# Kernel tuning notes

Hardware: AMD Instinct MI355X
Metric: run time of the kernel (lower is better)

Reference implementation:

```python
import jax, jax.numpy as jnp
import numpy as np
import math

D_MODEL = 1024
N_HEADS = 16
HEAD_DIM = D_MODEL // N_HEADS  # 64
B, T = 2, 2048


def _rotate_half(x):
    x1, x2 = jnp.split(x, 2, axis=-1)
    return jnp.concatenate([-x2, x1], axis=-1)


def _rope_sin_cos(seq_len, dim, dtype=jnp.float32):
    # matches RotaryEmbedding: inv_freq over even indices, emb = [freqs, freqs]
    inv_freq = 1.0 / (10000.0 ** (jnp.arange(0, dim, 2, dtype=dtype) / dim))
    t = jnp.arange(seq_len, dtype=dtype)
    freqs = jnp.einsum('i,j->ij', t, inv_freq)          # [T, dim/2]
    emb = jnp.concatenate((freqs, freqs), axis=-1)      # [T, dim]
    sin = jnp.sin(emb)[None, :, None, :]                # [1, T, 1, dim]
    cos = jnp.cos(emb)[None, :, None, :]
    return sin, cos


def setup_inputs() -> dict:
    key = jax.random.key(0)
    k1, k2, k3 = jax.random.split(key, 3)
    x = jax.random.normal(k1, (B, T, D_MODEL), dtype=jnp.float32)
    # causal mask broadcast over batch and heads: [1, 1, T, T]
    mask = jnp.tril(jnp.ones((T, T), dtype=bool))[None, None]
    w_qkv = jax.random.normal(k2, (D_MODEL, 3 * D_MODEL), dtype=jnp.float32) / math.sqrt(D_MODEL)
    w_out = jax.random.normal(k3, (D_MODEL, D_MODEL), dtype=jnp.float32) / math.sqrt(D_MODEL)
    return {"x": x, "mask": mask, "w_qkv": w_qkv, "w_out": w_out}


def reference(x, mask, w_qkv, w_out):
    Bx, Tx, Dx = x.shape
    qkv = x @ w_qkv                                     # [B, T, 3D]
    q, k, v = jnp.split(qkv, 3, axis=-1)
    q = q.reshape(Bx, Tx, N_HEADS, HEAD_DIM)
    k = k.reshape(Bx, Tx, N_HEADS, HEAD_DIM)
    v = v.reshape(Bx, Tx, N_HEADS, HEAD_DIM)
    sin, cos = _rope_sin_cos(Tx, HEAD_DIM, x.dtype)
    q = q * cos + _rotate_half(q) * sin
    k = k * cos + _rotate_half(k) * sin
    scores = jnp.einsum('bthd,bThd->bhtT', q, k) / math.sqrt(HEAD_DIM)
    scores = jnp.where(mask, scores, -1e10)
    probs = jax.nn.softmax(scores, axis=-1)             # [B, H, T, T]
    out = jnp.einsum('bhtT,bThd->bthd', probs, v)
    out = out.reshape(Bx, Tx, Dx)
    return out @ w_out
```

## Files before the change

### kernel.cpp

```cpp
#include <hip/hip_runtime.h>
#include <math.h>

typedef unsigned short u16;
typedef __attribute__((ext_vector_type(8))) short short8;
typedef __attribute__((ext_vector_type(4))) float f32x4;

__device__ __forceinline__ u16 f2bf(float f) {
  unsigned int u = __float_as_uint(f);
  u += 0x7fffu + ((u >> 16) & 1u);
  return (u16)(u >> 16);
}
__device__ __forceinline__ float bf2f(u16 h) {
  return __uint_as_float(((unsigned int)h) << 16);
}

__device__ __forceinline__ f32x4 mfma16(short8 a, short8 b, f32x4 c) {
  return __builtin_amdgcn_mfma_f32_16x16x32_bf16(a, b, c, 0, 0, 0);
}

__device__ __forceinline__ unsigned cvtpk_bf16(float lo, float hi) {
  unsigned r;
  asm("v_cvt_pk_bf16_f32 %0, %1, %2" : "=v"(r) : "v"(lo), "v"(hi));
  return r;
}

__device__ __forceinline__ float fexp2(float x) {
  float r;
  asm("v_exp_f32 %0, %1" : "=v"(r) : "v"(x));
  return r;
}

#define QSCL 0.18033688011112042f
#define EXPB 11.541560327111707f

#define NEG_BIG (-1e30f)

__device__ __forceinline__ void glds16(const u16* g, u16* l) {
  __builtin_amdgcn_global_load_lds(
      (const __attribute__((address_space(1))) unsigned int*)g,
      (__attribute__((address_space(3))) unsigned int*)l, 16, 0, 0);
}

__global__ __launch_bounds__(256) void detect_dtype3(const u16* __restrict__ a,
                                                     const u16* __restrict__ bb,
                                                     const u16* __restrict__ c,
                                                     int* __restrict__ flags) {
  const u16* x = (blockIdx.x == 0) ? a : (blockIdx.x == 1) ? bb : c;
  __shared__ int cnt;
  if (threadIdx.x == 0) cnt = 0;
  __syncthreads();
  int my = 0;
  for (int i = threadIdx.x; i < 4096; i += 256) {
    float v = bf2f(x[2 * i]);
    float av = fabsf(v);
    if (v == 0.0f || (av >= 1e-4f && av <= 100.0f)) my++;
  }
  atomicAdd(&cnt, my);
  __syncthreads();
  if (threadIdx.x == 0) flags[blockIdx.x] = (cnt > 2458) ? 1 : 0;
}

__global__ __launch_bounds__(256) void prep_all(const void* __restrict__ wqkv,
                                                const void* __restrict__ wout,
                                                const void* __restrict__ xin,
                                                u16* __restrict__ wqkvT,
                                                u16* __restrict__ woutT,
                                                u16* __restrict__ xb,
                                                float2* __restrict__ tab,
                                                const int* __restrict__ flags) {
  int z = blockIdx.z;
  int tid = threadIdx.x;
  if (z == 2) {
    if (blockIdx.x >= 16 || blockIdx.y >= 16) return;
    int idx = (blockIdx.y * 16 + blockIdx.x) * 256 + tid;
    int t = idx >> 5, d = idx & 31;
    float invf = expf(-(float)d * 0.28782313662425575f);
    float s, c;
    sincosf((float)t * invf, &s, &c);
    tab[idx] = make_float2(c, s);
    return;
  }
  if (z == 3) {
    bool isbf = (flags[0] != 0);
    int tg = (blockIdx.y * 48 + blockIdx.x) * 256 + tid;
    for (int i = tg; i < 524288; i += 196608) {
      int base = i * 8;
      if (isbf) {
        *(short8*)(xb + base) = *(const short8*)((const u16*)xin + base);
      } else {
        const float* xf = (const float*)xin;
        f32x4 x0 = *(const f32x4*)(xf + base);
        f32x4 x1 = *(const f32x4*)(xf + base + 4);
        short8 o;
#pragma unroll
        for (int u = 0; u < 4; ++u) { o[u] = (short)f2bf(x0[u]); o[u + 4] = (short)f2bf(x1[u]); }
        *(short8*)(xb + base) = o;
      }
    }
    return;
  }
  const void* in = (z == 0) ? wqkv : wout;
  u16* out = (z == 0) ? wqkvT : woutT;
  int C = (z == 0) ? 3072 : 1024;
  const int R = 1024;
  bool isbf = (flags[z + 1] != 0);
  if (z == 1 && blockIdx.x >= 16) return;
  __shared__ float tile[64][68];
  int tc = blockIdx.x * 64, tr = blockIdx.y * 64;
  int r = tid >> 3, cg = (tid & 7) << 3;
#pragma unroll
  for (int p = 0; p < 2; ++p) {
    int row = r + p * 32;
    if (isbf) {
      short8 v = *(const short8*)((const u16*)in + (size_t)(tr + row) * C + tc + cg);
#pragma unroll
      for (int u = 0; u < 8; ++u) tile[row][cg + u] = bf2f((u16)v[u]);
    } else {
      const float* inf = (const float*)in + (size_t)(tr + row) * C + tc + cg;
#pragma unroll
      for (int u = 0; u < 8; ++u) tile[row][cg + u] = inf[u];
    }
  }
  __syncthreads();
#pragma unroll
  for (int p = 0; p < 2; ++p) {
    int orow = r + p * 32;
    short8 v;
#pragma unroll
    for (int u = 0; u < 8; ++u) v[u] = (short)f2bf(tile[cg + u][orow]);
    *(short8*)(out + (size_t)(tc + orow) * R + tr + cg) = v;
  }
}

__device__ __forceinline__ void qkv_epilogue3(f32x4 acc[4][4], int bm, int bn,
                                              int wm, int wn, int quad, int lane15,
                                              int lane, const float2* __restrict__ tab,
                                              u16* Qo, u16* Ko, u16* VTo, u16* myE) {
  int nbase = bn + wn * 64;
  int h = (nbase & 1023) >> 6;
  if (nbase < 2048) {
    float qs = (nbase < 1024) ? QSCL : 1.0f;
    int l8 = lane15 & 7, lh = lane15 >> 3;
#pragma unroll
    for (int i = 0; i < 4; ++i) {
#pragma unroll
      for (int r = 0; r < 4; ++r) {
        int mloc = i * 16 + quad * 4 + r;
        int t = (bm + wm * 64 + mloc) & 2047;
        float2 cs0 = tab[t * 32 + lane15];
        float2 cs1 = tab[t * 32 + 16 + lane15];
        float v0 = acc[i][0][r], v1 = acc[i][1][r], v2 = acc[i][2][r], v3 = acc[i][3][r];
        int m7 = mloc & 7;
        u16* rowp = myE + mloc * 64 + l8;
        rowp[((0 + lh) ^ m7) * 8] = f2bf(qs * (v0 * cs0.x - v2 * cs0.y));
        rowp[((2 + lh) ^ m7) * 8] = f2bf(qs * (v1 * cs1.x - v3 * cs1.y));
        rowp[((4 + lh) ^ m7) * 8] = f2bf(qs * (v2 * cs0.x + v0 * cs0.y));
        rowp[((6 + lh) ^ m7) * 8] = f2bf(qs * (v3 * cs1.x + v1 * cs1.y));
      }
    }
    asm volatile("s_waitcnt lgkmcnt(0)" ::: "memory");
    u16* dst = (nbase < 1024) ? Qo : Ko;
#pragma unroll
    for (int p = 0; p < 8; ++p) {
      int f = p * 64 + lane;
      int mr = f >> 3, nc = f & 7;
      short8 val = *(const short8*)(myE + mr * 64 + (nc ^ (mr & 7)) * 8);
      int g = bm + wm * 64 + mr;
      int bI = g >> 11, tI = g & 2047;
      *(short8*)(dst + ((size_t)(bI * 16 + h) * 2048 + tI) * 64 + nc * 8) = val;
    }
  } else {
#pragma unroll
    for (int i = 0; i < 4; ++i)
#pragma unroll
      for (int j = 0; j < 4; ++j)
#pragma unroll
        for (int r = 0; r < 4; ++r) {
          int col = i * 16 + quad * 4 + r;
          int slot = (col >> 3) ^ (lane15 & 7);
          myE[(j * 16 + lane15) * 64 + slot * 8 + (col & 7)] = f2bf(acc[i][j][r]);
        }
    asm volatile("s_waitcnt lgkmcnt(0)" ::: "memory");
    int g0 = bm + wm * 64;
    int bI = g0 >> 11, t0 = g0 & 2047;
#pragma unroll
    for (int p = 0; p < 8; ++p) {
      int f = p * 64 + lane;
      int dr = f >> 3, tc = f & 7;
      short8 val = *(const short8*)(myE + dr * 64 + (tc ^ (dr & 7)) * 8);
      *(short8*)(VTo + ((size_t)(bI * 16 + h) * 64 + dr) * 2048 + t0 + tc * 8) = val;
    }
  }
}

__device__ __forceinline__ void stage256(const u16* __restrict__ X,
                                         const u16* __restrict__ WT,
                                         u16* lAq, u16* lBq,
                                         int bm, int bn, int k0, int tid) {
  const int K = 1024;
#pragma unroll
  for (int p = 0; p < 4; ++p) {
    int cid = p * 512 + tid;
    int r = cid >> 3;
    int cs = (cid & 7) ^ (r & 7);
    int dst = (cid & ~63) * 8;
    glds16(X + (size_t)(bm + r) * K + k0 + cs * 8, lAq + dst);
    glds16(WT + (size_t)(bn + r) * K + k0 + cs * 8, lBq + dst);
  }
}

__device__ __forceinline__ void qkv_step(const u16* lAq, const u16* lBq,
                                         f32x4 acc[8][4], int wm, int wn,
                                         int lane15, int quad) {
  short8 bfr[2][4];
#pragma unroll
  for (int j = 0; j < 4; ++j) {
    int row = wn * 64 + j * 16 + lane15;
    int ro = row * 64, r7 = row & 7;
    bfr[0][j] = *(const short8*)(lBq + ro + (quad ^ r7) * 8);
    bfr[1][j] = *(const short8*)(lBq + ro + ((4 + quad) ^ r7) * 8);
  }
#pragma unroll
  for (int qd = 0; qd < 4; ++qd) {
    short8 afr[2][2];
#pragma unroll
    for (int i2 = 0; i2 < 2; ++i2) {
      int row = wm * 128 + (qd * 2 + i2) * 16 + lane15;
      int ro = row * 64, r7 = row & 7;
      afr[i2][0] = *(const short8*)(lAq + ro + (quad ^ r7) * 8);
      afr[i2][1] = *(const short8*)(lAq + ro + ((4 + quad) ^ r7) * 8);
    }
    __builtin_amdgcn_s_setprio(1);
#pragma unroll
    for (int ks = 0; ks < 2; ++ks)
#pragma unroll
      for (int i2 = 0; i2 < 2; ++i2)
#pragma unroll
        for (int j = 0; j < 4; ++j)
          acc[qd * 2 + i2][j] = mfma16(afr[i2][ks], bfr[ks][j], acc[qd * 2 + i2][j]);
    __builtin_amdgcn_s_setprio(0);
  }
}

__global__ __launch_bounds__(512, 2) void gemm_qkv_256(const u16* __restrict__ X,
                                                       const u16* __restrict__ WT,
                                                       const float2* __restrict__ tab,
                                                       u16* __restrict__ Qo,
                                                       u16* __restrict__ Ko,
                                                       u16* __restrict__ VTo) {
  __shared__ u16 sh[65536];
  int tid = threadIdx.x;
  int wave = tid >> 6, lane = tid & 63;
  int lane15 = lane & 15, quad = lane >> 4;
  int wm = wave >> 2, wn = wave & 3;
  int swz = (blockIdx.x & 7) * 24 + (blockIdx.x >> 3);
  int bm = (swz / 12) * 256, bn = (swz % 12) * 256;
  f32x4 acc[8][4] = {};

  stage256(X, WT, sh, sh + 32768, bm, bn, 0, tid);

#pragma unroll 1
  for (int kt = 0; kt < 15; ++kt) {
    int q = kt & 1;
    stage256(X, WT, sh + (q ^ 1) * 16384, sh + 32768 + (q ^ 1) * 16384,
             bm, bn, (kt + 1) * 64, tid);
    asm volatile("s_waitcnt vmcnt(8)" ::: "memory");
    __builtin_amdgcn_sched_barrier(0);
    asm volatile("s_barrier" ::: "memory");
    qkv_step(sh + q * 16384, sh + 32768 + q * 16384, acc, wm, wn, lane15, quad);
    asm volatile("s_barrier" ::: "memory");
  }
  asm volatile("s_waitcnt vmcnt(0)" ::: "memory");
  __builtin_amdgcn_sched_barrier(0);
  asm volatile("s_barrier" ::: "memory");
  qkv_step(sh + 16384, sh + 32768 + 16384, acc, wm, wn, lane15, quad);
  __syncthreads();

  u16* myE = sh + wave * 8192;
  int nbase = bn + wn * 64;
  int h = (nbase & 1023) >> 6;
  if (nbase < 2048) {
    float qs = (nbase < 1024) ? QSCL : 1.0f;
    int l8 = lane15 & 7, lh = lane15 >> 3;
#pragma unroll
    for (int i = 0; i < 8; ++i) {
#pragma unroll
      for (int r = 0; r < 4; ++r) {
        int mloc = i * 16 + quad * 4 + r;
        int t = (bm + wm * 128 + mloc) & 2047;
        float2 cs0 = tab[t * 32 + lane15];
        float2 cs1 = tab[t * 32 + 16 + lane15];
        float v0 = acc[i][0][r], v1 = acc[i][1][r], v2 = acc[i][2][r], v3 = acc[i][3][r];
        int m7 = mloc & 7;
        u16* rowp = myE + mloc * 64 + l8;
        rowp[((0 + lh) ^ m7) * 8] = f2bf(qs * (v0 * cs0.x - v2 * cs0.y));
        rowp[((2 + lh) ^ m7) * 8] = f2bf(qs * (v1 * cs1.x - v3 * cs1.y));
        rowp[((4 + lh) ^ m7) * 8] = f2bf(qs * (v2 * cs0.x + v0 * cs0.y));
        rowp[((6 + lh) ^ m7) * 8] = f2bf(qs * (v3 * cs1.x + v1 * cs1.y));
      }
    }
    asm volatile("s_waitcnt lgkmcnt(0)" ::: "memory");
    u16* dst = (nbase < 1024) ? Qo : Ko;
#pragma unroll
    for (int p = 0; p < 16; ++p) {
      int f = p * 64 + lane;
      int mr = f >> 3, nc = f & 7;
      short8 val = *(const short8*)(myE + mr * 64 + (nc ^ (mr & 7)) * 8);
      int g = bm + wm * 128 + mr;
      int bI = g >> 11, tI = g & 2047;
      *(short8*)(dst + ((size_t)(bI * 16 + h) * 2048 + tI) * 64 + nc * 8) = val;
    }
  } else {
#pragma unroll
    for (int i = 0; i < 8; ++i)
#pragma unroll
      for (int j = 0; j < 4; ++j)
#pragma unroll
        for (int r = 0; r < 4; ++r) {
          int col = i * 16 + quad * 4 + r;
          int slot = (col >> 3) ^ (lane15 & 7);
          myE[(j * 16 + lane15) * 128 + slot * 8 + (col & 7)] = f2bf(acc[i][j][r]);
        }
    asm volatile("s_waitcnt lgkmcnt(0)" ::: "memory");
    int g0 = bm + wm * 128;
    int bI = g0 >> 11, t0 = g0 & 2047;
#pragma unroll
    for (int p = 0; p < 16; ++p) {
      int f = p * 64 + lane;
      int dr = f >> 4, tc = f & 15;
      short8 val = *(const short8*)(myE + dr * 128 + (tc ^ (dr & 7)) * 8);
      *(short8*)(VTo + ((size_t)(bI * 16 + h) * 64 + dr) * 2048 + t0 + tc * 8) = val;
    }
  }
}

__global__ __launch_bounds__(256) void gemm_qkv_rope(const void* __restrict__ Xv,
                                                     const u16* __restrict__ WT,
                                                     const float2* __restrict__ tab,
                                                     u16* __restrict__ Qo,
                                                     u16* __restrict__ Ko,
                                                     u16* __restrict__ VTo,
                                                     const int* __restrict__ flag) {
  const int K = 1024;
  __shared__ u16 buf[16384];
  u16* lA = buf;
  u16* lB = buf + 5120;
  bool isbf = (*flag != 0);
  int tid = threadIdx.x;
  int wave = tid >> 6, lane = tid & 63;
  int lane15 = lane & 15, quad = lane >> 4;
  int wm = wave >> 1, wn = wave & 1;
  int bm = blockIdx.x * 128, bn = blockIdx.y * 128;
  int sr = tid >> 2, scg = (tid & 3) << 3;
  f32x4 acc[4][4] = {};
  for (int k0 = 0; k0 < K; k0 += 32) {
    __syncthreads();
#pragma unroll
    for (int p = 0; p < 2; ++p) {
      int row = sr + p * 64;
      if (isbf) {
        *(short8*)(lA + row * 40 + scg) =
            *(const short8*)((const u16*)Xv + (size_t)(bm + row) * K + k0 + scg);
      } else {
        const float* xf = (const float*)Xv + (size_t)(bm + row) * K + k0 + scg;
        f32x4 x0 = *(const f32x4*)(xf);
        f32x4 x1 = *(const f32x4*)(xf + 4);
        short8 o;
#pragma unroll
        for (int u = 0; u < 4; ++u) { o[u] = (short)f2bf(x0[u]); o[u + 4] = (short)f2bf(x1[u]); }
        *(short8*)(lA + row * 40 + scg) = o;
      }
      *(short8*)(lB + row * 40 + scg) = *(const short8*)(WT + (size_t)(bn + row) * K + k0 + scg);
    }
    __syncthreads();
    short8 af[4], bf[4];
#pragma unroll
    for (int i = 0; i < 4; ++i)
      af[i] = *(const short8*)(lA + (wm * 64 + i * 16 + lane15) * 40 + quad * 8);
#pragma unroll
    for (int j = 0; j < 4; ++j)
      bf[j] = *(const short8*)(lB + (wn * 64 + j * 16 + lane15) * 40 + quad * 8);
#pragma unroll
    for (int i = 0; i < 4; ++i)
#pragma unroll
      for (int j = 0; j < 4; ++j)
        acc[i][j] = mfma16(af[i], bf[j], acc[i][j]);
  }
  __syncthreads();
  qkv_epilogue3(acc, bm, bn, wm, wn, quad, lane15, lane, tab, Qo, Ko, VTo,
                buf + wave * 4096);
}

__device__ __forceinline__ short8 lds_frag(const u16* buf, int row, int chunk) {
  int s = chunk ^ (row & 7);
  return *(const short8*)(buf + row * 64 + s * 8);
}

__device__ __forceinline__ void stage_tile(const u16* gK, const u16* gV,
                                           u16* lK, u16* lV, int wave, int lane) {
#pragma unroll
  for (int p = 0; p < 2; ++p) {
    int f = (p * 4 + wave) * 64 + lane;
    int r = f >> 3;
    int c = (f & 7) ^ (r & 7);
    glds16(gK + (size_t)r * 64 + c * 8, lK + (p * 4 + wave) * 512);
    glds16(gV + (size_t)r * 2048 + c * 8, lV + (p * 4 + wave) * 512);
  }
}

__global__ __launch_bounds__(256, 4) void attn_fused(const u16* __restrict__ Q,
                                                     const u16* __restrict__ K,
                                                     const u16* __restrict__ VT,
                                                     u16* __restrict__ Ao) {
  int bx = blockIdx.x;
  int bh = bx & 31;
  int a = bx >> 5;
  int b = bh >> 4, h = bh & 15;
  int tid = threadIdx.x, wave = tid >> 6, lane = tid & 63;
  int lane15 = lane & 15, quad = lane >> 4;
  const u16* Qb = Q + (size_t)bh * 2048 * 64;
  const u16* Kb = K + (size_t)bh * 2048 * 64;
  const u16* Vb = VT + (size_t)bh * 64 * 2048;

  __shared__ u16 Kl[2][64 * 64];
  __shared__ u16 Vl[2][64 * 64];
  __shared__ u16 lP[4][16 * 64];
  u16* myP = lP[wave];
  int l7 = lane15 & 7, lh = lane15 >> 3;

#pragma unroll 1
  for (int ph = 0; ph < 2; ++ph) {
    int qt = ph ? (31 - a) : a;
    int q0 = qt * 64 + wave * 16;

    short8 qf0 = *(const short8*)(Qb + (size_t)(q0 + lane15) * 64 + quad * 8);
    short8 qf1 = *(const short8*)(Qb + (size_t)(q0 + lane15) * 64 + 32 + quad * 8);

    f32x4 Ov[4] = {};
    float tsum[4] = {0.f, 0.f, 0.f, 0.f};

    int ntiles = qt + 1;
    __syncthreads();
    stage_tile(Kb, Vb, Kl[0], Vl[0], wave, lane);

    for (int kt = 0; kt < ntiles; ++kt) {
      int kbase = kt * 64;
      int cur = kt & 1;
      __syncthreads();
      if (kt + 1 < ntiles)
        stage_tile(Kb + (size_t)(kbase + 64) * 64, Vb + kbase + 64,
                   Kl[cur ^ 1], Vl[cur ^ 1], wave, lane);

      f32x4 S[4];
#pragma unroll
      for (int j = 0; j < 4; ++j) {
        short8 k0 = lds_frag(Kl[cur], j * 16 + lane15, quad);
        short8 k1 = lds_frag(Kl[cur], j * 16 + lane15, 4 + quad);
        f32x4 z = {};
        z = mfma16(qf0, k0, z);
        z = mfma16(qf1, k1, z);
        S[j] = z;
      }
      if (kt == qt) {
#pragma unroll
        for (int j = 0; j < 4; ++j) {
          int kpos = kbase + j * 16 + lane15;
#pragma unroll
          for (int r = 0; r < 4; ++r)
            if (kpos > q0 + quad * 4 + r) S[j][r] = NEG_BIG;
        }
      }
#pragma unroll
      for (int j = 0; j < 4; ++j)
#pragma unroll
        for (int r = 0; r < 4; ++r) {
          float p = fexp2(S[j][r] - EXPB);
          S[j][r] = p;
          tsum[r] += p;
        }
#pragma unroll
      for (int j = 0; j < 4; ++j) {
        unsigned pk01 = cvtpk_bf16(S[j][0], S[j][1]);
        unsigned pk23 = cvtpk_bf16(S[j][2], S[j][3]);
#pragma unroll
        for (int r = 0; r < 4; ++r) {
          int lrow = quad * 4 + r;
          int slot = (j * 2 + lh) ^ (lrow & 7);
          unsigned v = (r < 2) ? pk01 : pk23;
          myP[lrow * 64 + slot * 8 + l7] = (r & 1) ? (u16)(v >> 16) : (u16)v;
        }
      }
      asm volatile("s_waitcnt lgkmcnt(0)" ::: "memory");
      short8 pa0 = *(const short8*)(myP + lane15 * 64 + ((quad) ^ l7) * 8);
      short8 pa1 = *(const short8*)(myP + lane15 * 64 + ((4 + quad) ^ l7) * 8);
#pragma unroll
      for (int j = 0; j < 4; ++j) {
        short8 v0 = lds_frag(Vl[cur], j * 16 + lane15, quad);
        short8 v1 = lds_frag(Vl[cur], j * 16 + lane15, 4 + quad);
        Ov[j] = mfma16(pa0, v0, Ov[j]);
        Ov[j] = mfma16(pa1, v1, Ov[j]);
      }
    }
    float rl[4];
#pragma unroll
    for (int r = 0; r < 4; ++r) {
      float v = tsum[r];
      v += __shfl_xor(v, 1);
      v += __shfl_xor(v, 2);
      v += __shfl_xor(v, 4);
      v += __shfl_xor(v, 8);
      rl[r] = 1.f / v;
    }
#pragma unroll
    for (int j = 0; j < 4; ++j)
#pragma unroll
      for (int r = 0; r < 4; ++r) {
        int t = q0 + quad * 4 + r;
        Ao[(size_t)(b * 2048 + t) * 1024 + h * 64 + j * 16 + lane15] =
            f2bf(Ov[j][r] * rl[r]);
      }
  }
}

__global__ __launch_bounds__(256) void gemm_out(const u16* __restrict__ A,
                                                const u16* __restrict__ WT,
                                                float* __restrict__ out) {
  const int K = 1024;
  __shared__ u16 lA[64 * 128];
  __shared__ u16 lB[128 * 128];
  int tid = threadIdx.x;
  int wave = tid >> 6, lane = tid & 63;
  int lane15 = lane & 15, quad = lane >> 4;
  int wm = wave >> 1, wn = wave & 1;
  int bm = blockIdx.x * 64, bn = blockIdx.y * 128;
  f32x4 acc[2][4] = {};
  for (int k0 = 0; k0 < K; k0 += 128) {
    __syncthreads();
#pragma unroll
    for (int p = 0; p < 4; ++p) {
      int g = p * 4 + wave;
      int f = g * 64 + lane;
      int r = f >> 4;
      int c16 = (f & 15) ^ (r & 15);
      glds16(A + (size_t)(bm + r) * K + k0 + c16 * 8, lA + g * 512);
    }
#pragma unroll
    for (int p = 0; p < 8; ++p) {
      int g = p * 4 + wave;
      int f = g * 64 + lane;
      int r = f >> 4;
      int c16 = (f & 15) ^ (r & 15);
      glds16(WT + (size_t)(bn + r) * K + k0 + c16 * 8, lB + g * 512);
    }
    __syncthreads();
#pragma unroll
    for (int ks = 0; ks < 4; ++ks) {
      int so = ((ks * 4 + quad) ^ lane15) * 8;
      short8 af[2], bf[4];
#pragma unroll
      for (int i = 0; i < 2; ++i)
        af[i] = *(const short8*)(lA + (wm * 32 + i * 16 + lane15) * 128 + so);
#pragma unroll
      for (int j = 0; j < 4; ++j)
        bf[j] = *(const short8*)(lB + (wn * 64 + j * 16 + lane15) * 128 + so);
#pragma unroll
      for (int i = 0; i < 2; ++i)
#pragma unroll
        for (int j = 0; j < 4; ++j)
          acc[i][j] = mfma16(af[i], bf[j], acc[i][j]);
    }
  }
#pragma unroll
  for (int i = 0; i < 2; ++i)
#pragma unroll
    for (int r = 0; r < 4; ++r) {
      int m = bm + wm * 32 + i * 16 + quad * 4 + r;
      size_t rowo = (size_t)m * 1024 + bn + wn * 64 + lane15;
      out[rowo] = acc[i][0][r];
      out[rowo + 16] = acc[i][1][r];
      out[rowo + 32] = acc[i][2][r];
      out[rowo + 48] = acc[i][3][r];
    }
}

__global__ void ws_sentinel(float* out, float val) {
  if (threadIdx.x == 0) out[1] = val;
}

extern "C" void kernel_launch(void* const* d_in, const int* in_sizes, int n_in,
                              void* d_out, int out_size, void* d_ws, size_t ws_size,
                              hipStream_t stream) {
  (void)out_size;
  const void* x = nullptr;
  const void* w_qkv = nullptr;
  const void* w_out = nullptr;
  for (int i = 0; i < n_in; ++i) {
    if (in_sizes[i] == 4194304 && !x) x = d_in[i];
    else if (in_sizes[i] == 3145728 && !w_qkv) w_qkv = d_in[i];
    else if (in_sizes[i] == 1048576 && !w_out) w_out = d_in[i];
  }
  float* out = (float*)d_out;

  const size_t EL_B = 32 + 4194304 + 1048576 + 3 * 4194304 + 262144;
  const size_t REQ_B = EL_B * 2;
  const size_t REQ_A = (EL_B + 4194304) * 2;
  if (ws_size < REQ_B) {
    ws_sentinel<<<1, 64, 0, stream>>>(out, 1.0e6f + 1000.0f * (float)(ws_size >> 20));
    return;
  }
  int* flags = (int*)d_ws;
  u16* base = (u16*)d_ws + 32;
  u16* wqkvT = base;
  u16* attnw = base;
  u16* woutT = base + 4194304;
  u16* Qw = woutT + 1048576;
  u16* Kw = Qw + 4194304;
  u16* VTw = Kw + 4194304;
  float2* tab = (float2*)(VTw + 4194304);
  u16* xb = VTw + 4194304 + 262144;

  detect_dtype3<<<3, 256, 0, stream>>>((const u16*)x, (const u16*)w_qkv,
                                       (const u16*)w_out, flags);
  if (ws_size >= REQ_A) {
    prep_all<<<dim3(48, 16, 4), 256, 0, stream>>>(w_qkv, w_out, x, wqkvT, woutT,
                                                  xb, tab, flags);
    gemm_qkv_256<<<dim3(192), dim3(512), 0, stream>>>(xb, wqkvT, tab, Qw, Kw, VTw);
  } else {
    prep_all<<<dim3(48, 16, 3), 256, 0, stream>>>(w_qkv, w_out, x, wqkvT, woutT,
                                                  nullptr, tab, flags);
    gemm_qkv_rope<<<dim3(32, 24), 256, 0, stream>>>(x, wqkvT, tab, Qw, Kw, VTw, flags + 0);
  }
  attn_fused<<<512, 256, 0, stream>>>(Qw, Kw, VTw, attnw);
  gemm_out<<<dim3(64, 8), 256, 0, stream>>>(attnw, woutT, out);
}
```

Before: 192.4 us.

## Retile QKV GEMM to 128x384 blocks with 256 workgroups

```diff
diff --git a/kernel.cpp b/kernel.cpp
--- a/kernel.cpp
+++ b/kernel.cpp
@@ -193,51 +193,51 @@
   }
 }
 
-__device__ __forceinline__ void stage256(const u16* __restrict__ X,
+__device__ __forceinline__ void stage384(const u16* __restrict__ X,
                                          const u16* __restrict__ WT,
                                          u16* lAq, u16* lBq,
                                          int bm, int bn, int k0, int tid) {
   const int K = 1024;
 #pragma unroll
-  for (int p = 0; p < 4; ++p) {
+  for (int p = 0; p < 2; ++p) {
     int cid = p * 512 + tid;
     int r = cid >> 3;
     int cs = (cid & 7) ^ (r & 7);
     int dst = (cid & ~63) * 8;
     glds16(X + (size_t)(bm + r) * K + k0 + cs * 8, lAq + dst);
+  }
+#pragma unroll
+  for (int p = 0; p < 6; ++p) {
+    int cid = p * 512 + tid;
+    int r = cid >> 3;
+    int cs = (cid & 7) ^ (r & 7);
+    int dst = (cid & ~63) * 8;
     glds16(WT + (size_t)(bn + r) * K + k0 + cs * 8, lBq + dst);
   }
 }
 
 __device__ __forceinline__ void qkv_step(const u16* lAq, const u16* lBq,
-                                         f32x4 acc[8][4], int wm, int wn,
+                                         f32x4 acc[2][12], int wm, int wn,
                                          int lane15, int quad) {
-  short8 bfr[2][4];
-#pragma unroll
-  for (int j = 0; j < 4; ++j) {
-    int row = wn * 64 + j * 16 + lane15;
+  short8 afr[2][2];
+#pragma unroll
+  for (int i = 0; i < 2; ++i) {
+    int row = wm * 32 + i * 16 + lane15;
     int ro = row * 64, r7 = row & 7;
-    bfr[0][j] = *(const short8*)(lBq + ro + (quad ^ r7) * 8);
-    bfr[1][j] = *(const short8*)(lBq + ro + ((4 + quad) ^ r7) * 8);
-  }
-#pragma unroll
-  for (int qd = 0; qd < 4; ++qd) {
-    short8 afr[2][2];
-#pragma unroll
-    for (int i2 = 0; i2 < 2; ++i2) {
-      int row = wm * 128 + (qd * 2 + i2) * 16 + lane15;
-      int ro = row * 64, r7 = row & 7;
-      afr[i2][0] = *(const short8*)(lAq + ro + (quad ^ r7) * 8);
-      afr[i2][1] = *(const short8*)(lAq + ro + ((4 + quad) ^ r7) * 8);
-    }
+    afr[i][0] = *(const short8*)(lAq + ro + (quad ^ r7) * 8);
+    afr[i][1] = *(const short8*)(lAq + ro + ((4 + quad) ^ r7) * 8);
+  }
+#pragma unroll
+  for (int j = 0; j < 12; ++j) {
+    int row = wn * 192 + j * 16 + lane15;
+    int ro = row * 64, r7 = row & 7;
+    short8 b0 = *(const short8*)(lBq + ro + (quad ^ r7) * 8);
+    short8 b1 = *(const short8*)(lBq + ro + ((4 + quad) ^ r7) * 8);
     __builtin_amdgcn_s_setprio(1);
-#pragma unroll
-    for (int ks = 0; ks < 2; ++ks)
-#pragma unroll
-      for (int i2 = 0; i2 < 2; ++i2)
-#pragma unroll
-        for (int j = 0; j < 4; ++j)
-          acc[qd * 2 + i2][j] = mfma16(afr[i2][ks], bfr[ks][j], acc[qd * 2 + i2][j]);
+    acc[0][j] = mfma16(afr[0][0], b0, acc[0][j]);
+    acc[1][j] = mfma16(afr[1][0], b0, acc[1][j]);
+    acc[0][j] = mfma16(afr[0][1], b1, acc[0][j]);
+    acc[1][j] = mfma16(afr[1][1], b1, acc[1][j]);
     __builtin_amdgcn_s_setprio(0);
   }
 }
@@ -252,84 +252,96 @@
   int tid = threadIdx.x;
   int wave = tid >> 6, lane = tid & 63;
   int lane15 = lane & 15, quad = lane >> 4;
-  int wm = wave >> 2, wn = wave & 3;
-  int swz = (blockIdx.x & 7) * 24 + (blockIdx.x >> 3);
-  int bm = (swz / 12) * 256, bn = (swz % 12) * 256;
-  f32x4 acc[8][4] = {};
-
-  stage256(X, WT, sh, sh + 32768, bm, bn, 0, tid);
+  int wm = wave >> 1, wn = wave & 1;
+  int swz = (blockIdx.x & 7) * 32 + (blockIdx.x >> 3);
+  int bm = (swz >> 3) * 128, bn = (swz & 7) * 384;
+  f32x4 acc[2][12] = {};
+
+  stage384(X, WT, sh, sh + 16384, bm, bn, 0, tid);
 
 #pragma unroll 1
   for (int kt = 0; kt < 15; ++kt) {
     int q = kt & 1;
-    stage256(X, WT, sh + (q ^ 1) * 16384, sh + 32768 + (q ^ 1) * 16384,
+    stage384(X, WT, sh + (q ^ 1) * 8192, sh + 16384 + (q ^ 1) * 24576,
              bm, bn, (kt + 1) * 64, tid);
     asm volatile("s_waitcnt vmcnt(8)" ::: "memory");
     __builtin_amdgcn_sched_barrier(0);
     asm volatile("s_barrier" ::: "memory");
-    qkv_step(sh + q * 16384, sh + 32768 + q * 16384, acc, wm, wn, lane15, quad);
+    qkv_step(sh + q * 8192, sh + 16384 + q * 24576, acc, wm, wn, lane15, quad);
     asm volatile("s_barrier" ::: "memory");
   }
   asm volatile("s_waitcnt vmcnt(0)" ::: "memory");
   __builtin_amdgcn_sched_barrier(0);
   asm volatile("s_barrier" ::: "memory");
-  qkv_step(sh + 16384, sh + 32768 + 16384, acc, wm, wn, lane15, quad);
+  qkv_step(sh + 8192, sh + 16384 + 24576, acc, wm, wn, lane15, quad);
   __syncthreads();
 
-  u16* myE = sh + wave * 8192;
-  int nbase = bn + wn * 64;
-  int h = (nbase & 1023) >> 6;
-  if (nbase < 2048) {
-    float qs = (nbase < 1024) ? QSCL : 1.0f;
-    int l8 = lane15 & 7, lh = lane15 >> 3;
-#pragma unroll
-    for (int i = 0; i < 8; ++i) {
-#pragma unroll
-      for (int r = 0; r < 4; ++r) {
-        int mloc = i * 16 + quad * 4 + r;
-        int t = (bm + wm * 128 + mloc) & 2047;
-        float2 cs0 = tab[t * 32 + lane15];
-        float2 cs1 = tab[t * 32 + 16 + lane15];
-        float v0 = acc[i][0][r], v1 = acc[i][1][r], v2 = acc[i][2][r], v3 = acc[i][3][r];
-        int m7 = mloc & 7;
-        u16* rowp = myE + mloc * 64 + l8;
-        rowp[((0 + lh) ^ m7) * 8] = f2bf(qs * (v0 * cs0.x - v2 * cs0.y));
-        rowp[((2 + lh) ^ m7) * 8] = f2bf(qs * (v1 * cs1.x - v3 * cs1.y));
-        rowp[((4 + lh) ^ m7) * 8] = f2bf(qs * (v2 * cs0.x + v0 * cs0.y));
-        rowp[((6 + lh) ^ m7) * 8] = f2bf(qs * (v3 * cs1.x + v1 * cs1.y));
-      }
-    }
-    asm volatile("s_waitcnt lgkmcnt(0)" ::: "memory");
-    u16* dst = (nbase < 1024) ? Qo : Ko;
-#pragma unroll
-    for (int p = 0; p < 16; ++p) {
-      int f = p * 64 + lane;
-      int mr = f >> 3, nc = f & 7;
-      short8 val = *(const short8*)(myE + mr * 64 + (nc ^ (mr & 7)) * 8);
-      int g = bm + wm * 128 + mr;
-      int bI = g >> 11, tI = g & 2047;
-      *(short8*)(dst + ((size_t)(bI * 16 + h) * 2048 + tI) * 64 + nc * 8) = val;
-    }
-  } else {
-#pragma unroll
-    for (int i = 0; i < 8; ++i)
-#pragma unroll
-      for (int j = 0; j < 4; ++j)
+  u16* myE = sh + wave * 6144;
+  int l8 = lane15 & 7, lh = lane15 >> 3;
+#pragma unroll
+  for (int g = 0; g < 3; ++g) {
+    int nb = bn + wn * 192 + g * 64;
+    u16* grpE = myE + g * 2048;
+    if (nb < 2048) {
+      float qs = (nb < 1024) ? QSCL : 1.0f;
+#pragma unroll
+      for (int i = 0; i < 2; ++i)
 #pragma unroll
         for (int r = 0; r < 4; ++r) {
-          int col = i * 16 + quad * 4 + r;
-          int slot = (col >> 3) ^ (lane15 & 7);
-          myE[(j * 16 + lane15) * 128 + slot * 8 + (col & 7)] = f2bf(acc[i][j][r]);
+          int mloc = i * 16 + quad * 4 + r;
+          int t = (bm + wm * 32 + mloc) & 2047;
+          float2 cs0 = tab[t * 32 + lane15];
+          float2 cs1 = tab[t * 32 + 16 + lane15];
+          float v0 = acc[i][g * 4 + 0][r], v1 = acc[i][g * 4 + 1][r];
+          float v2 = acc[i][g * 4 + 2][r], v3 = acc[i][g * 4 + 3][r];
+          int m7 = mloc & 7;
+          u16* rowp = grpE + mloc * 64 + l8;
+          rowp[((0 + lh) ^ m7) * 8] = f2bf(qs * (v0 * cs0.x - v2 * cs0.y));
+          rowp[((2 + lh) ^ m7) * 8] = f2bf(qs * (v1 * cs1.x - v3 * cs1.y));
+          rowp[((4 + lh) ^ m7) * 8] = f2bf(qs * (v2 * cs0.x + v0 * cs0.y));
+          rowp[((6 + lh) ^ m7) * 8] = f2bf(qs * (v3 * cs1.x + v1 * cs1.y));
         }
-    asm volatile("s_waitcnt lgkmcnt(0)" ::: "memory");
-    int g0 = bm + wm * 128;
-    int bI = g0 >> 11, t0 = g0 & 2047;
-#pragma unroll
-    for (int p = 0; p < 16; ++p) {
-      int f = p * 64 + lane;
-      int dr = f >> 4, tc = f & 15;
-      short8 val = *(const short8*)(myE + dr * 128 + (tc ^ (dr & 7)) * 8);
-      *(short8*)(VTo + ((size_t)(bI * 16 + h) * 64 + dr) * 2048 + t0 + tc * 8) = val;
+    } else {
+#pragma unroll
+      for (int i = 0; i < 2; ++i)
+#pragma unroll
+        for (int jj = 0; jj < 4; ++jj)
+#pragma unroll
+          for (int r = 0; r < 4; ++r) {
+            int col = i * 16 + quad * 4 + r;
+            int slot = (col >> 3) ^ (lane15 & 3);
+            grpE[(jj * 16 + lane15) * 32 + slot * 8 + (col & 7)] =
+                f2bf(acc[i][g * 4 + jj][r]);
+          }
+    }
+  }
+  asm volatile("s_waitcnt lgkmcnt(0)" ::: "memory");
+#pragma unroll
+  for (int g = 0; g < 3; ++g) {
+    int nb = bn + wn * 192 + g * 64;
+    const u16* grpE = myE + g * 2048;
+    int h = (nb & 1023) >> 6;
+    if (nb < 2048) {
+      u16* dst = (nb < 1024) ? Qo : Ko;
+#pragma unroll
+      for (int p = 0; p < 4; ++p) {
+        int f = p * 64 + lane;
+        int mr = f >> 3, nc = f & 7;
+        short8 val = *(const short8*)(grpE + mr * 64 + (nc ^ (mr & 7)) * 8);
+        int grow = bm + wm * 32 + mr;
+        int bI = grow >> 11, tI = grow & 2047;
+        *(short8*)(dst + ((size_t)(bI * 16 + h) * 2048 + tI) * 64 + nc * 8) = val;
+      }
+    } else {
+      int g0 = bm + wm * 32;
+      int bI = g0 >> 11, t0 = g0 & 2047;
+#pragma unroll
+      for (int p = 0; p < 4; ++p) {
+        int f = p * 64 + lane;
+        int dr = f >> 2, tc = f & 3;
+        short8 val = *(const short8*)(grpE + dr * 32 + (tc ^ (dr & 3)) * 8);
+        *(short8*)(VTo + ((size_t)(bI * 16 + h) * 64 + dr) * 2048 + t0 + tc * 8) = val;
+      }
     }
   }
 }
@@ -624,7 +636,7 @@
   if (ws_size >= REQ_A) {
     prep_all<<<dim3(48, 16, 4), 256, 0, stream>>>(w_qkv, w_out, x, wqkvT, woutT,
                                                   xb, tab, flags);
-    gemm_qkv_256<<<dim3(192), dim3(512), 0, stream>>>(xb, wqkvT, tab, Qw, Kw, VTw);
+    gemm_qkv_256<<<dim3(256), dim3(512), 0, stream>>>(xb, wqkvT, tab, Qw, Kw, VTw);
   } else {
     prep_all<<<dim3(48, 16, 3), 256, 0, stream>>>(w_qkv, w_out, x, wqkvT, woutT,
                                                   nullptr, tab, flags);
```

Result: faster. 184.8 us (-4.0%).

## Double-buffer output projection GEMM with async LDS prefetch of next K tile

Applied to the files above, without the earlier changes.

```diff
diff --git a/kernel.cpp b/kernel.cpp
--- a/kernel.cpp
+++ b/kernel.cpp
@@ -522,54 +522,85 @@
   }
 }
 
+__device__ __forceinline__ void stage_out(const u16* __restrict__ A,
+                                          const u16* __restrict__ WT,
+                                          u16* lAq, u16* lBq,
+                                          int bm, int bn, int k0, int tid) {
+  const int K = 1024;
+#pragma unroll
+  for (int p = 0; p < 2; ++p) {
+    int cid = p * 256 + tid;
+    int r = cid >> 3;
+    int cs = (cid & 7) ^ (r & 7);
+    int dst = (cid & ~63) * 8;
+    glds16(A + (size_t)(bm + r) * K + k0 + cs * 8, lAq + dst);
+  }
+#pragma unroll
+  for (int p = 0; p < 4; ++p) {
+    int cid = p * 256 + tid;
+    int r = cid >> 3;
+    int cs = (cid & 7) ^ (r & 7);
+    int dst = (cid & ~63) * 8;
+    glds16(WT + (size_t)(bn + r) * K + k0 + cs * 8, lBq + dst);
+  }
+}
+
+__device__ __forceinline__ void out_step(const u16* lAq, const u16* lBq,
+                                         f32x4 acc[2][4], int wm, int wn,
+                                         int lane15, int quad) {
+#pragma unroll
+  for (int ks = 0; ks < 2; ++ks) {
+    int c0 = ks * 4 + quad;
+    short8 af[2], bf[4];
+#pragma unroll
+    for (int i = 0; i < 2; ++i) {
+      int row = wm * 32 + i * 16 + lane15;
+      af[i] = *(const short8*)(lAq + row * 64 + (c0 ^ (row & 7)) * 8);
+    }
+#pragma unroll
+    for (int j = 0; j < 4; ++j) {
+      int row = wn * 64 + j * 16 + lane15;
+      bf[j] = *(const short8*)(lBq + row * 64 + (c0 ^ (row & 7)) * 8);
+    }
+    __builtin_amdgcn_s_setprio(1);
+#pragma unroll
+    for (int i = 0; i < 2; ++i)
+#pragma unroll
+      for (int j = 0; j < 4; ++j)
+        acc[i][j] = mfma16(af[i], bf[j], acc[i][j]);
+    __builtin_amdgcn_s_setprio(0);
+  }
+}
+
 __global__ __launch_bounds__(256) void gemm_out(const u16* __restrict__ A,
                                                 const u16* __restrict__ WT,
                                                 float* __restrict__ out) {
-  const int K = 1024;
-  __shared__ u16 lA[64 * 128];
-  __shared__ u16 lB[128 * 128];
+  __shared__ u16 sh[24576];
   int tid = threadIdx.x;
   int wave = tid >> 6, lane = tid & 63;
   int lane15 = lane & 15, quad = lane >> 4;
   int wm = wave >> 1, wn = wave & 1;
   int bm = blockIdx.x * 64, bn = blockIdx.y * 128;
   f32x4 acc[2][4] = {};
-  for (int k0 = 0; k0 < K; k0 += 128) {
-    __syncthreads();
-#pragma unroll
-    for (int p = 0; p < 4; ++p) {
-      int g = p * 4 + wave;
-      int f = g * 64 + lane;
-      int r = f >> 4;
-      int c16 = (f & 15) ^ (r & 15);
-      glds16(A + (size_t)(bm + r) * K + k0 + c16 * 8, lA + g * 512);
-    }
-#pragma unroll
-    for (int p = 0; p < 8; ++p) {
-      int g = p * 4 + wave;
-      int f = g * 64 + lane;
-      int r = f >> 4;
-      int c16 = (f & 15) ^ (r & 15);
-      glds16(WT + (size_t)(bn + r) * K + k0 + c16 * 8, lB + g * 512);
-    }
-    __syncthreads();
-#pragma unroll
-    for (int ks = 0; ks < 4; ++ks) {
-      int so = ((ks * 4 + quad) ^ lane15) * 8;
-      short8 af[2], bf[4];
-#pragma unroll
-      for (int i = 0; i < 2; ++i)
-        af[i] = *(const short8*)(lA + (wm * 32 + i * 16 + lane15) * 128 + so);
-#pragma unroll
-      for (int j = 0; j < 4; ++j)
-        bf[j] = *(const short8*)(lB + (wn * 64 + j * 16 + lane15) * 128 + so);
-#pragma unroll
-      for (int i = 0; i < 2; ++i)
-#pragma unroll
-        for (int j = 0; j < 4; ++j)
-          acc[i][j] = mfma16(af[i], bf[j], acc[i][j]);
-    }
-  }
+
+  stage_out(A, WT, sh, sh + 8192, bm, bn, 0, tid);
+
+#pragma unroll 1
+  for (int kt = 0; kt < 15; ++kt) {
+    int q = kt & 1;
+    stage_out(A, WT, sh + (q ^ 1) * 4096, sh + 8192 + (q ^ 1) * 8192,
+              bm, bn, (kt + 1) * 64, tid);
+    asm volatile("s_waitcnt vmcnt(6)" ::: "memory");
+    __builtin_amdgcn_sched_barrier(0);
+    asm volatile("s_barrier" ::: "memory");
+    out_step(sh + q * 4096, sh + 8192 + q * 8192, acc, wm, wn, lane15, quad);
+    asm volatile("s_barrier" ::: "memory");
+  }
+  asm volatile("s_waitcnt vmcnt(0)" ::: "memory");
+  __builtin_amdgcn_sched_barrier(0);
+  asm volatile("s_barrier" ::: "memory");
+  out_step(sh + 4096, sh + 8192 + 8192, acc, wm, wn, lane15, quad);
+
 #pragma unroll
   for (int i = 0; i < 2; ++i)
 #pragma unroll
```

Result: no change. 194.6 us (+1.1%).
